# Optimization experiments

Hardware: AMD Instinct MI355X
Metric: run time of the kernel (lower is better)

## Reference

```python
import jax, jax.numpy as jnp
import numpy as np

B, S, D = 1, 1024, 512
HEADS, HID = 8, 64
DH = D // HEADS          # 64
CD = D * DH              # 32768 channels in diagonal block
DT = 0.1


def causal_fft_conv(u, k):
    # u: (..., C, S), k: (C, S) -> causal convolution along last axis
    s = u.shape[-1]
    n = 2 * s
    Uf = jnp.fft.rfft(u, n=n, axis=-1)
    Kf = jnp.fft.rfft(k, n=n, axis=-1)
    return jnp.fft.irfft(Uf * Kf, n=n, axis=-1)[..., :s]


def setup_inputs() -> dict:
    key = jax.random.key(0)
    ks = jax.random.split(key, 10)
    x = jax.random.normal(ks[0], (B, S, D), dtype=jnp.float32)
    sc = 1.0 / np.sqrt(D)
    WQ = jax.random.normal(ks[1], (D, D), dtype=jnp.float32) * sc
    WK = jax.random.normal(ks[2], (D, D), dtype=jnp.float32) * sc
    WV = jax.random.normal(ks[3], (D, D), dtype=jnp.float32) * sc
    WO = jax.random.normal(ks[4], (D, D), dtype=jnp.float32) * sc
    # shift SSM: taps C (A = shift matrix, B = e1) + skip D
    C_shift = jax.random.normal(ks[5], (D, HID), dtype=jnp.float32) / np.sqrt(HID)
    D_shift = jax.random.normal(ks[6], (D,), dtype=jnp.float32)
    # S4D-Inv initialization (deterministic: real_random=imag_random=False)
    n = np.arange(HID, dtype=np.float32)
    A_re = jnp.full((HID,), -0.5, dtype=jnp.float32)
    A_im = jnp.asarray((HID / np.pi) * (HID / (2.0 * n + 1.0) - 1.0), dtype=jnp.float32)
    C_re = jax.random.normal(ks[7], (CD, HID), dtype=jnp.float32) / np.sqrt(HID)
    C_im = jax.random.normal(ks[8], (CD, HID), dtype=jnp.float32) / np.sqrt(HID)
    D_diag = jax.random.normal(ks[9], (CD,), dtype=jnp.float32)
    return {"x": x, "WQ": WQ, "WK": WK, "WV": WV, "WO": WO,
            "C_shift": C_shift, "D_shift": D_shift,
            "A_re": A_re, "A_im": A_im, "C_re": C_re, "C_im": C_im,
            "D_diag": D_diag}


def reference(x, WQ, WK, WV, WO, C_shift, D_shift, A_re, A_im, C_re, C_im, D_diag):
    b, s, d = x.shape
    Q = x @ WQ.T
    K = x @ WK.T
    V = x @ WV.T

    # ---- S4 shift block on K: FIR conv with taps C_shift + skip ----
    k_shift = jnp.pad(C_shift, ((0, 0), (0, s - HID)))  # (D, S)
    Kc = jnp.swapaxes(K, 1, 2)                          # (B, D, S)
    Kc = causal_fft_conv(Kc, k_shift) + D_shift[:, None] * Kc
    K = jnp.swapaxes(Kc, 1, 2)

    # ---- heads ----
    Qh = jnp.swapaxes(Q.reshape(b, s, HEADS, DH), 1, 2)  # (B,H,S,dh)
    Kh = jnp.swapaxes(K.reshape(b, s, HEADS, DH), 1, 2)
    Vh = jnp.swapaxes(V.reshape(b, s, HEADS, DH), 1, 2)

    # KV outer product: (B,H,S,dh,dh)
    KV = Kh[..., :, None] * Vh[..., None, :]
    KVf = jnp.transpose(KV, (0, 2, 1, 3, 4)).reshape(b, s, CD)

    # ---- S4D diagonal block (bilinear disc., convolutional form) ----
    A = A_re + 1j * A_im                                # (N,) complex
    dA = (1.0 + DT * A / 2.0) / (1.0 - DT * A / 2.0)
    dB = DT / (1.0 - DT * A / 2.0)
    logdA = jnp.log(dA)                                 # (N,)
    vand = jnp.exp(jnp.arange(s)[None, :] * logdA[:, None])  # (N, S)
    CB = (C_re + 1j * C_im) * dB[None, :]               # (CD, N)
    Kd = 2.0 * jnp.real(CB @ vand)                      # (CD, S) SSM kernel

    KVc = jnp.swapaxes(KVf, 1, 2)                       # (B, CD, S)
    KVc = causal_fft_conv(KVc, Kd) + D_diag[:, None] * KVc
    KVd = jnp.swapaxes(KVc, 1, 2).reshape(b, s, HEADS, DH, DH)
    KVd = jnp.transpose(KVd, (0, 2, 1, 3, 4))           # (B,H,S,dh,dh)

    # ---- combine with Q and output projection ----
    O = jnp.einsum('bhnc,bhncd->bhnd', Qh, KVd)         # (B,H,S,dh)
    O = jnp.swapaxes(O, 1, 2).reshape(b, s, d)
    return O @ WO.T
```

## Files before the change

### kernel.cpp

```cpp
#include <hip/hip_runtime.h>

#define S 1024
#define D 512
#define HID 64
#define CD 32768
#define DT 0.1f

typedef __attribute__((ext_vector_type(4))) float floatx4;
typedef __attribute__((ext_vector_type(8))) short shortx8;
typedef short shortx8_a __attribute__((ext_vector_type(8), may_alias));
typedef short shortx4_a __attribute__((ext_vector_type(4), may_alias));
typedef unsigned int uint_a __attribute__((may_alias));
typedef unsigned int uint2_a __attribute__((ext_vector_type(2), may_alias));
typedef unsigned int uint4_a __attribute__((ext_vector_type(4), may_alias));
typedef float float4_a __attribute__((ext_vector_type(4), may_alias));
typedef float float_a __attribute__((may_alias));

__device__ __forceinline__ unsigned short f2bf(float f) {
  union { float f; unsigned int u; } v;
  v.f = f;
  unsigned int r = v.u + 0x7FFFu + ((v.u >> 16) & 1u);
  return (unsigned short)(r >> 16);
}
__device__ __forceinline__ float bf2f(unsigned short h) {
  union { unsigned int u; float f; } v;
  v.u = ((unsigned int)h) << 16;
  return v.f;
}
__device__ __forceinline__ void cvt_hilo(float v, unsigned short& h, unsigned short& lo) {
  h = f2bf(v);
  lo = f2bf(v - bf2f(h));
}

__global__ __launch_bounds__(256) void fused_qkv_cbkd(
    const float* __restrict__ x, const float* __restrict__ WQ,
    const float* __restrict__ WK, const float* __restrict__ WV,
    const float* __restrict__ Are, const float* __restrict__ Aim,
    const float* __restrict__ Cre, const float* __restrict__ Cim,
    float* __restrict__ QT, float* __restrict__ KrawT, float* __restrict__ VT,
    unsigned short* __restrict__ cb2pack, unsigned short* __restrict__ kdpack) {
  __shared__ __align__(16) char LB[21760];
  const int tid = threadIdx.x;
  const int bid = blockIdx.x;
  const int l = tid & 63, w = tid >> 6;
  const int l15 = l & 15, q = l >> 4;

  if (bid < 384) {
    unsigned short* Wh = (unsigned short*)LB;
    unsigned short* Wl = Wh + 2560;
    unsigned short* Xh = Wl + 2560;
    unsigned short* Xl = Xh + 2560;
    float_a* Ct = (float_a*)LB;
    const int mat = bid >> 7;
    const int rem = bid & 127;
    const int n0 = (rem & 7) * 64, m0 = (rem >> 3) * 64;
    const float* Wsel = (mat == 0) ? WQ : (mat == 1) ? WK : WV;
    float* CT = (mat == 0) ? QT : (mat == 1) ? KrawT : VT;

    floatx4 acc[4];
#pragma unroll
    for (int nt = 0; nt < 4; ++nt) acc[nt] = (floatx4){0.f, 0.f, 0.f, 0.f};

    for (int k0 = 0; k0 < D; k0 += 32) {
      if (k0) __syncthreads();
#pragma unroll
      for (int p = 0; p < 2; ++p) {
        const int idx = tid + 256 * p;
        const int row = idx >> 3, c4 = (idx & 7) * 4;
        const float4 wv = *(const float4*)&Wsel[(n0 + row) * D + k0 + c4];
        const float4 xv = *(const float4*)&x[(m0 + row) * D + k0 + c4];
        unsigned short h0, h1, h2, h3, g0, g1, g2, g3;
        cvt_hilo(wv.x, h0, g0); cvt_hilo(wv.y, h1, g1);
        cvt_hilo(wv.z, h2, g2); cvt_hilo(wv.w, h3, g3);
        uint2_a hv = {(unsigned int)h0 | ((unsigned int)h1 << 16),
                      (unsigned int)h2 | ((unsigned int)h3 << 16)};
        uint2_a lv = {(unsigned int)g0 | ((unsigned int)g1 << 16),
                      (unsigned int)g2 | ((unsigned int)g3 << 16)};
        *(uint2_a*)&Wh[row * 40 + c4] = hv;
        *(uint2_a*)&Wl[row * 40 + c4] = lv;
        cvt_hilo(xv.x, h0, g0); cvt_hilo(xv.y, h1, g1);
        cvt_hilo(xv.z, h2, g2); cvt_hilo(xv.w, h3, g3);
        uint2_a hv2 = {(unsigned int)h0 | ((unsigned int)h1 << 16),
                       (unsigned int)h2 | ((unsigned int)h3 << 16)};
        uint2_a lv2 = {(unsigned int)g0 | ((unsigned int)g1 << 16),
                       (unsigned int)g2 | ((unsigned int)g3 << 16)};
        *(uint2_a*)&Xh[row * 40 + c4] = hv2;
        *(uint2_a*)&Xl[row * 40 + c4] = lv2;
      }
      __syncthreads();
      const shortx8 xh = *(const shortx8_a*)&Xh[(16 * w + l15) * 40 + 8 * q];
      const shortx8 xl = *(const shortx8_a*)&Xl[(16 * w + l15) * 40 + 8 * q];
#pragma unroll
      for (int nt = 0; nt < 4; ++nt) {
        const shortx8 wh = *(const shortx8_a*)&Wh[(16 * nt + l15) * 40 + 8 * q];
        const shortx8 wl = *(const shortx8_a*)&Wl[(16 * nt + l15) * 40 + 8 * q];
        acc[nt] = __builtin_amdgcn_mfma_f32_16x16x32_bf16(wh, xh, acc[nt], 0, 0, 0);
        acc[nt] = __builtin_amdgcn_mfma_f32_16x16x32_bf16(wh, xl, acc[nt], 0, 0, 0);
        acc[nt] = __builtin_amdgcn_mfma_f32_16x16x32_bf16(wl, xh, acc[nt], 0, 0, 0);
      }
    }
    __syncthreads();
#pragma unroll
    for (int nt = 0; nt < 4; ++nt)
#pragma unroll
      for (int v = 0; v < 4; ++v)
        Ct[(16 * nt + 4 * q + v) * 68 + 16 * w + l15] = acc[nt][v];
    __syncthreads();
#pragma unroll
    for (int p = 0; p < 4; ++p) {
      const int row = (tid >> 4) + 16 * p;
      const int col4 = (tid & 15) * 4;
      *(float4_a*)&CT[(n0 + row) * S + m0 + col4] = *(const float4_a*)&Ct[row * 68 + col4];
    }
  } else {
    unsigned short* cbs = (unsigned short*)LB;
    unsigned short* PCc2s = (unsigned short*)(LB + 4352);
    const int c0 = (bid - 384) << 4;
    {
      const int n = l, seg = w;
      const float ar = Are[n], ai = Aim[n];
      const float den_re = 1.0f - 0.05f * ar;
      const float den_im = -0.05f * ai;
      const float num_re = 1.0f + 0.05f * ar;
      const float num_im = 0.05f * ai;
      const float inv_d2 = 1.0f / (den_re * den_re + den_im * den_im);
      const float dAr = (num_re * den_re + num_im * den_im) * inv_d2;
      const float dAi = (num_im * den_re - num_re * den_im) * inv_d2;
      float e2r = dAr * dAr - dAi * dAi, e2i = 2.0f * dAr * dAi;
      float e4r = e2r * e2r - e2i * e2i, e4i = 2.0f * e2r * e2i;
      float e8r = e4r * e4r - e4i * e4i, e8i = 2.0f * e4r * e4i;
      float e16r = e8r * e8r - e8i * e8i, e16i = 2.0f * e8r * e8i;
      float br = 1.0f, bi = 0.0f;
      for (int sgo = 0; sgo < seg; ++sgo) {
        const float nr = br * e16r - bi * e16i;
        bi = br * e16i + bi * e16r;
        br = nr;
      }
      float pr = br, pi = bi;
      for (int k = 16 * seg + 1; k <= 16 * seg + 16; ++k) {
        const float nr = pr * dAr - pi * dAi;
        pi = pr * dAi + pi * dAr;
        pr = nr;
        if (k <= 63) {
          PCc2s[k * 136 + n] = f2bf(pr);
          PCc2s[k * 136 + 64 + n] = f2bf(-pi);
        }
      }
      if (seg == 0) {
        PCc2s[n] = f2bf(1.0f);
        PCc2s[64 + n] = 0;
      }
    }
#pragma unroll
    for (int ii = 0; ii < 4; ++ii) {
      const int idx = tid + 256 * ii;
      const int ci = idx >> 6, n = idx & 63;
      const int c = c0 + ci;
      const float ar = Are[n], ai = Aim[n];
      const float den_re = 1.0f - 0.05f * ar;
      const float den_im = -0.05f * ai;
      const float inv_d2 = 1.0f / (den_re * den_re + den_im * den_im);
      const float dBr = DT * den_re * inv_d2;
      const float dBi = -DT * den_im * inv_d2;
      const float cr = Cre[c * HID + n], cim = Cim[c * HID + n];
      const unsigned short re = f2bf(2.0f * (cr * dBr - cim * dBi));
      const unsigned short im = f2bf(2.0f * (cr * dBi + cim * dBr));
      cbs[ci * 136 + n] = re;
      cbs[ci * 136 + 64 + n] = im;
      cb2pack[c * 128 + n] = re;
      cb2pack[c * 128 + 64 + n] = im;
    }
    __syncthreads();
    floatx4 acc = {0.f, 0.f, 0.f, 0.f};
#pragma unroll
    for (int k = 0; k < 4; ++k) {
      const shortx8 a = *(const shortx8_a*)&cbs[l15 * 136 + 8 * q + 32 * k];
      const shortx8 b = *(const shortx8_a*)&PCc2s[(16 * w + l15) * 136 + 8 * q + 32 * k];
      acc = __builtin_amdgcn_mfma_f32_16x16x32_bf16(a, b, acc, 0, 0, 0);
    }
    const int dlt = 16 * w + l15;
#pragma unroll
    for (int v = 0; v < 4; ++v)
      kdpack[(c0 + 4 * q + v) * 128 + 64 - dlt] = f2bf(acc[v]);
    const int row = tid >> 4, p = tid & 15;
#pragma unroll
    for (int k2 = 0; k2 < 4; ++k2) {
      const int idx = p + 16 * k2;
      const int m = (idx == 0) ? 0 : 64 + idx;
      kdpack[(c0 + row) * 128 + m] = 0;
    }
  }
}

__global__ __launch_bounds__(256) void shift_ssmT(const float* __restrict__ KrawT,
                                                  const float* __restrict__ Cs,
                                                  const float* __restrict__ Ds,
                                                  float* __restrict__ KnT) {
  __shared__ float kpad[64 + S];
  const int d = blockIdx.x, tid = threadIdx.x;
  if (tid < 64) kpad[tid] = 0.0f;
  *(float4_a*)&kpad[64 + 4 * tid] = *(const float4_a*)&KrawT[d * S + 4 * tid];
  const float dskip = Ds[d];
  const float* taps = Cs + d * HID;
  __syncthreads();
  float acc[4];
#pragma unroll
  for (int s = 0; s < 4; ++s) acc[s] = dskip * kpad[64 + tid + 256 * s];
  for (int j = 0; j < 64; ++j) {
    const float tj = taps[j];
#pragma unroll
    for (int s = 0; s < 4; ++s) acc[s] += tj * kpad[64 + tid + 256 * s - j];
  }
#pragma unroll
  for (int s = 0; s < 4; ++s) KnT[d * S + tid + 256 * s] = acc[s];
}

__global__ __launch_bounds__(256, 2) void s4d_fused(
    const float* __restrict__ KnT, const float* __restrict__ VT,
    const float* __restrict__ QT,
    const float* __restrict__ Are, const float* __restrict__ Aim,
    const unsigned short* __restrict__ cb2pack,
    const unsigned short* __restrict__ kdpack,
    const float* __restrict__ Dd, float* __restrict__ OT) {
  __shared__ __align__(16) unsigned short SHu[18176];
  const int tid = threadIdx.x;
  const int l = tid & 63, w = tid >> 6;
  const int l15 = l & 15, q = l >> 4;
  const int h = blockIdx.x >> 6, j = blockIdx.x & 63;
  const int dv = (h << 6) + j;

  {
    const int n = l, seg = w;
    unsigned short* PAreW = SHu;
    unsigned short* PAimW = SHu + 4608;
    unsigned short* PCcW = SHu + 9216;
    float_a* dA64W = (float_a*)(SHu + 17920);
    const float ar = Are[n], ai = Aim[n];
    const float den_re = 1.0f - 0.05f * ar;
    const float den_im = -0.05f * ai;
    const float num_re = 1.0f + 0.05f * ar;
    const float num_im = 0.05f * ai;
    const float inv_d2 = 1.0f / (den_re * den_re + den_im * den_im);
    const float dAr = (num_re * den_re + num_im * den_im) * inv_d2;
    const float dAi = (num_im * den_re - num_re * den_im) * inv_d2;
    float e2r = dAr * dAr - dAi * dAi, e2i = 2.0f * dAr * dAi;
    float e4r = e2r * e2r - e2i * e2i, e4i = 2.0f * e2r * e2i;
    float e8r = e4r * e4r - e4i * e4i, e8i = 2.0f * e4r * e4i;
    float e16r = e8r * e8r - e8i * e8i, e16i = 2.0f * e8r * e8i;
    float br = 1.0f, bi = 0.0f;
    for (int sgo = 0; sgo < seg; ++sgo) {
      const float nr = br * e16r - bi * e16i;
      bi = br * e16i + bi * e16r;
      br = nr;
    }
    float pr = br, pi = bi;
    for (int k = 16 * seg + 1; k <= 16 * seg + 16; ++k) {
      const float nr = pr * dAr - pi * dAi;
      pi = pr * dAi + pi * dAr;
      pr = nr;
      if (k <= 63) {
        PAreW[n * 72 + 63 - k] = f2bf(pr);
        PAimW[n * 72 + 63 - k] = f2bf(pi);
      }
      PCcW[(k - 1) * 136 + 2 * n] = f2bf(pr);
      PCcW[(k - 1) * 136 + 2 * n + 1] = f2bf(-pi);
      if (k == 64) {
        dA64W[2 * n] = pr;
        dA64W[2 * n + 1] = pi;
      }
    }
    if (seg == 0) {
      PAreW[n * 72 + 63] = f2bf(1.0f);
      PAimW[n * 72 + 63] = 0;
    }
  }
  float4 vvr[4];
#pragma unroll
  for (int s = 0; s < 4; ++s)
    vvr[s] = *(const float4*)&VT[dv * S + 4 * l + 256 * s];

  float c2r, c2i, dd;
  unsigned int kdv;
  {
    const int c = (h << 12) + (w << 6) + j;
    c2r = bf2f(cb2pack[c * 128 + l]);
    c2i = bf2f(cb2pack[c * 128 + 64 + l]);
    kdv = *(const uint_a*)&kdpack[c * 128 + 2 * l];
    dd = Dd[c];
  }
  __syncthreads();

  const unsigned short* PAre = SHu;
  const unsigned short* PAim = SHu + 4608;
  const unsigned short* PCc = SHu + 9216;
  const float_a* dA64v = (const float_a*)(SHu + 17920);
  const float er = dA64v[2 * l], ei = dA64v[2 * l + 1];
  shortx8 paR[4][2], paI[4][2];
#pragma unroll
  for (int tt = 0; tt < 4; ++tt) {
    const int rowb = (tt * 16 + l15) * 72 + 8 * q;
    paR[tt][0] = *(const shortx8_a*)&PAre[rowb];
    paR[tt][1] = *(const shortx8_a*)&PAre[rowb + 32];
    paI[tt][0] = *(const shortx8_a*)&PAim[rowb];
    paI[tt][1] = *(const shortx8_a*)&PAim[rowb + 32];
  }
  shortx8 pcb[4][4];
#pragma unroll
  for (int k = 0; k < 4; ++k)
#pragma unroll
    for (int tt = 0; tt < 4; ++tt)
      pcb[k][tt] = *(const shortx8_a*)&PCc[(tt * 16 + l15) * 136 + 8 * q + 32 * k];
  __syncthreads();

  unsigned short* WB = SHu + w * 4048;
  unsigned short* Ub = WB;
  unsigned short* SXY = WB + 1152;
  uint_a* kdR32 = (uint_a*)(WB + 3328);
  unsigned short* kdSH = WB + 3472;

  floatx4 OaccD[4];
  float4 Odd[4];
#pragma unroll
  for (int tt = 0; tt < 4; ++tt) OaccD[tt] = (floatx4){0.f, 0.f, 0.f, 0.f};
#pragma unroll
  for (int s = 0; s < 4; ++s) Odd[s] = make_float4(0.f, 0.f, 0.f, 0.f);

#pragma unroll 1
  for (int it = 0; it < 16; ++it) {
    float nc2r = 0.f, nc2i = 0.f, ndd = 0.f;
    unsigned int nkdv = 0;
    if (it < 15) {
      const int c = (h << 12) + (((it + 1) * 4 + w) << 6) + j;
      nc2r = bf2f(cb2pack[c * 128 + l]);
      nc2i = bf2f(cb2pack[c * 128 + 64 + l]);
      nkdv = *(const uint_a*)&kdpack[c * 128 + 2 * l];
      ndd = Dd[c];
    }
    const int dk = (h << 6) + it * 4 + w;
    const int kb = dk * S + 4 * l;
    float4 kx[4], qtv[4];
#pragma unroll
    for (int s = 0; s < 4; ++s) {
      kx[s] = *(const float4*)&KnT[kb + 256 * s];
      qtv[s] = *(const float4*)&QT[kb + 256 * s];
    }

    kdR32[l] = kdv;
    if (l < 4) kdR32[64 + l] = 0;
    asm volatile("" ::: "memory");
#pragma unroll
    for (int s2 = 0; s2 < 4; ++s2) {
      unsigned int v;
      if (s2 == 0) {
        v = kdR32[l];
      } else if (s2 == 1) {
        v = (kdR32[l] >> 16) | (kdR32[l + 1] << 16);
      } else if (s2 == 2) {
        v = kdR32[l + 1];
      } else {
        v = (kdR32[l + 1] >> 16) | (kdR32[l + 2] << 16);
      }
      *(uint_a*)&kdSH[s2 * 136 + 2 * l] = v;
    }
    asm volatile("" ::: "memory");

#pragma unroll
    for (int s = 0; s < 4; ++s) {
      const int t = 4 * l + 256 * s;
      const int g = t >> 6, r = t & 63;
      const float ux = kx[s].x * vvr[s].x;
      const float uy = kx[s].y * vvr[s].y;
      const float uz = kx[s].z * vvr[s].z;
      const float uw = kx[s].w * vvr[s].w;
      uint2_a pp;
      pp.x = (unsigned int)f2bf(ux) | ((unsigned int)f2bf(uy) << 16);
      pp.y = (unsigned int)f2bf(uz) | ((unsigned int)f2bf(uw) << 16);
      *(uint2_a*)&Ub[g * 72 + r] = pp;
      Odd[s].x += dd * qtv[s].x * ux;
      Odd[s].y += dd * qtv[s].y * uy;
      Odd[s].z += dd * qtv[s].z * uz;
      Odd[s].w += dd * qtv[s].w * uw;
    }
    asm volatile("" ::: "memory");

    const shortx8 b0 = *(const shortx8_a*)&Ub[l15 * 72 + 8 * q];
    const shortx8 b1 = *(const shortx8_a*)&Ub[l15 * 72 + 8 * q + 32];
#pragma unroll
    for (int tt = 0; tt < 4; ++tt) {
      floatx4 z = {0.f, 0.f, 0.f, 0.f};
      floatx4 sre = __builtin_amdgcn_mfma_f32_16x16x32_bf16(paR[tt][0], b0, z, 0, 0, 0);
      sre = __builtin_amdgcn_mfma_f32_16x16x32_bf16(paR[tt][1], b1, sre, 0, 0, 0);
      floatx4 sim = __builtin_amdgcn_mfma_f32_16x16x32_bf16(paI[tt][0], b0, z, 0, 0, 0);
      sim = __builtin_amdgcn_mfma_f32_16x16x32_bf16(paI[tt][1], b1, sim, 0, 0, 0);
      uint4_a wv;
      wv[0] = (unsigned int)f2bf(sre[0]) | ((unsigned int)f2bf(sim[0]) << 16);
      wv[1] = (unsigned int)f2bf(sre[1]) | ((unsigned int)f2bf(sim[1]) << 16);
      wv[2] = (unsigned int)f2bf(sre[2]) | ((unsigned int)f2bf(sim[2]) << 16);
      wv[3] = (unsigned int)f2bf(sre[3]) | ((unsigned int)f2bf(sim[3]) << 16);
      *(uint4_a*)&SXY[l15 * 136 + 32 * tt + 8 * q] = wv;
    }
    asm volatile("" ::: "memory");

    {
      unsigned int rdv[16];
#pragma unroll
      for (int g = 0; g < 16; ++g) rdv[g] = *(const uint_a*)&SXY[g * 136 + 2 * l];
      float xr = 0.f, xi = 0.f;
#pragma unroll
      for (int g = 0; g < 16; ++g) {
        *(uint_a*)&SXY[g * 136 + 2 * l] =
            (unsigned int)f2bf(c2r * xr - c2i * xi) |
            ((unsigned int)f2bf(c2r * xi + c2i * xr) << 16);
        union { unsigned int u; float f; } lo, hi;
        lo.u = rdv[g] << 16;
        hi.u = rdv[g] & 0xffff0000u;
        const float nr = er * xr - ei * xi + lo.f;
        xi = er * xi + ei * xr + hi.f;
        xr = nr;
      }
    }
    asm volatile("" ::: "memory");

    float qD[16];
    {
      const int qb = dk * S + 256 * q + l15;
#pragma unroll
      for (int tt = 0; tt < 4; ++tt)
#pragma unroll
        for (int v = 0; v < 4; ++v)
          qD[4 * tt + v] = QT[qb + 64 * v + 16 * tt];
    }

    floatx4 acc[4];
#pragma unroll
    for (int tt = 0; tt < 4; ++tt) acc[tt] = (floatx4){0.f, 0.f, 0.f, 0.f};
#pragma unroll
    for (int k = 0; k < 4; ++k) {
      const shortx8 xa = *(const shortx8_a*)&SXY[l15 * 136 + 8 * q + 32 * k];
#pragma unroll
      for (int tt = 0; tt < 4; ++tt)
        acc[tt] = __builtin_amdgcn_mfma_f32_16x16x32_bf16(xa, pcb[k][tt], acc[tt], 0, 0, 0);
    }
#pragma unroll
    for (int k = 0; k < 2; ++k) {
      const shortx8 ua = (k == 0) ? b0 : b1;
#pragma unroll
      for (int tt = 0; tt < 4; ++tt) {
        const int r = tt * 16 + l15;
        const int sSh = (4 - (r & 3)) & 3;
        const int addr = sSh * 136 + (64 - r - sSh) + 8 * q + 32 * k;
        const shortx4_a lo = *(const shortx4_a*)&kdSH[addr];
        const shortx4_a hi = *(const shortx4_a*)&kdSH[addr + 4];
        const shortx8 kb8 = __builtin_shufflevector(lo, hi, 0, 1, 2, 3, 4, 5, 6, 7);
        acc[tt] = __builtin_amdgcn_mfma_f32_16x16x32_bf16(ua, kb8, acc[tt], 0, 0, 0);
      }
    }
#pragma unroll
    for (int tt = 0; tt < 4; ++tt)
#pragma unroll
      for (int v = 0; v < 4; ++v)
        OaccD[tt][v] += qD[4 * tt + v] * acc[tt][v];
    c2r = nc2r; c2i = nc2i; kdv = nkdv; dd = ndd;
  }

  asm volatile("" ::: "memory");
  {
    float_a* Ored = (float_a*)WB;
#pragma unroll
    for (int tt = 0; tt < 4; ++tt)
#pragma unroll
      for (int v = 0; v < 4; ++v)
        Ored[256 * q + 64 * v + 16 * tt + l15 + q] = OaccD[tt][v];
    asm volatile("" ::: "memory");
    float4 Oa[4];
#pragma unroll
    for (int s = 0; s < 4; ++s) {
      const float4_a y4 = *(const float4_a*)&Ored[4 * l + 257 * s];
      Oa[s].x = y4.x + Odd[s].x;
      Oa[s].y = y4.y + Odd[s].y;
      Oa[s].z = y4.z + Odd[s].z;
      Oa[s].w = y4.w + Odd[s].w;
    }
    asm volatile("" ::: "memory");
#pragma unroll
    for (int s = 0; s < 4; ++s) {
      float4_a vv = {Oa[s].x, Oa[s].y, Oa[s].z, Oa[s].w};
      *(float4_a*)&Ored[4 * l + 256 * s] = vv;
    }
  }
  __syncthreads();
  {
    const int tq = 256 * w + 4 * l;
    float4_a acc = {0.f, 0.f, 0.f, 0.f};
#pragma unroll
    for (int w2 = 0; w2 < 4; ++w2) {
      const float_a* Ow2 = (const float_a*)(SHu + w2 * 4048);
      acc += *(const float4_a*)&Ow2[tq];
    }
    *(float4_a*)&OT[dv * S + tq] = acc;
  }
}

__global__ __launch_bounds__(256) void gemm_outT(const float* __restrict__ OT,
                                                 const float* __restrict__ WO,
                                                 float* __restrict__ out) {
  __shared__ __align__(16) char LB[20480];
  unsigned short* Wh = (unsigned short*)LB;
  unsigned short* Wl = Wh + 2560;
  unsigned short* Xh = Wl + 2560;
  unsigned short* Xl = Xh + 2560;
  float_a* Ct = (float_a*)LB;
  const int tid = threadIdx.x;
  const int l = tid & 63, w = tid >> 6;
  const int l15 = l & 15, q = l >> 4;
  const int n0 = (blockIdx.x & 7) * 64, m0 = (blockIdx.x >> 3) * 64;

  floatx4 acc[4];
#pragma unroll
  for (int nt = 0; nt < 4; ++nt) acc[nt] = (floatx4){0.f, 0.f, 0.f, 0.f};

  for (int k0 = 0; k0 < D; k0 += 32) {
    if (k0) __syncthreads();
#pragma unroll
    for (int p = 0; p < 2; ++p) {
      const int idx = tid + 256 * p;
      {
        const int row = idx >> 3, c4 = (idx & 7) * 4;
        const float4 wv = *(const float4*)&WO[(n0 + row) * D + k0 + c4];
        unsigned short h0, h1, h2, h3, g0, g1, g2, g3;
        cvt_hilo(wv.x, h0, g0); cvt_hilo(wv.y, h1, g1);
        cvt_hilo(wv.z, h2, g2); cvt_hilo(wv.w, h3, g3);
        uint2_a hv = {(unsigned int)h0 | ((unsigned int)h1 << 16),
                      (unsigned int)h2 | ((unsigned int)h3 << 16)};
        uint2_a lv = {(unsigned int)g0 | ((unsigned int)g1 << 16),
                      (unsigned int)g2 | ((unsigned int)g3 << 16)};
        *(uint2_a*)&Wh[row * 40 + c4] = hv;
        *(uint2_a*)&Wl[row * 40 + c4] = lv;
      }
      {
        const int kk = idx >> 4, m4 = (idx & 15) * 4;
        const float4 ov = *(const float4*)&OT[(k0 + kk) * S + m0 + m4];
        unsigned short h, g;
        cvt_hilo(ov.x, h, g); Xh[(m4 + 0) * 40 + kk] = h; Xl[(m4 + 0) * 40 + kk] = g;
        cvt_hilo(ov.y, h, g); Xh[(m4 + 1) * 40 + kk] = h; Xl[(m4 + 1) * 40 + kk] = g;
        cvt_hilo(ov.z, h, g); Xh[(m4 + 2) * 40 + kk] = h; Xl[(m4 + 2) * 40 + kk] = g;
        cvt_hilo(ov.w, h, g); Xh[(m4 + 3) * 40 + kk] = h; Xl[(m4 + 3) * 40 + kk] = g;
      }
    }
    __syncthreads();
    const shortx8 xh = *(const shortx8_a*)&Xh[(16 * w + l15) * 40 + 8 * q];
    const shortx8 xl = *(const shortx8_a*)&Xl[(16 * w + l15) * 40 + 8 * q];
#pragma unroll
    for (int nt = 0; nt < 4; ++nt) {
      const shortx8 wh = *(const shortx8_a*)&Wh[(16 * nt + l15) * 40 + 8 * q];
      const shortx8 wl = *(const shortx8_a*)&Wl[(16 * nt + l15) * 40 + 8 * q];
      acc[nt] = __builtin_amdgcn_mfma_f32_16x16x32_bf16(wh, xh, acc[nt], 0, 0, 0);
      acc[nt] = __builtin_amdgcn_mfma_f32_16x16x32_bf16(wh, xl, acc[nt], 0, 0, 0);
      acc[nt] = __builtin_amdgcn_mfma_f32_16x16x32_bf16(wl, xh, acc[nt], 0, 0, 0);
    }
  }
  __syncthreads();
#pragma unroll
  for (int nt = 0; nt < 4; ++nt)
#pragma unroll
    for (int v = 0; v < 4; ++v)
      Ct[(16 * w + l15) * 68 + 16 * nt + 4 * q + v] = acc[nt][v];
  __syncthreads();
#pragma unroll
  for (int p = 0; p < 4; ++p) {
    const int row = (tid >> 4) + 16 * p;
    const int col4 = (tid & 15) * 4;
    *(float4_a*)&out[(m0 + row) * D + n0 + col4] = *(const float4_a*)&Ct[row * 68 + col4];
  }
}

extern "C" void kernel_launch(void* const* d_in, const int* in_sizes, int n_in,
                              void* d_out, int out_size, void* d_ws, size_t ws_size,
                              hipStream_t stream) {
  const float* x   = (const float*)d_in[0];
  const float* WQ  = (const float*)d_in[1];
  const float* WK  = (const float*)d_in[2];
  const float* WV  = (const float*)d_in[3];
  const float* WO  = (const float*)d_in[4];
  const float* Cs  = (const float*)d_in[5];
  const float* Ds  = (const float*)d_in[6];
  const float* Are = (const float*)d_in[7];
  const float* Aim = (const float*)d_in[8];
  const float* Cre = (const float*)d_in[9];
  const float* Cim = (const float*)d_in[10];
  const float* Dd  = (const float*)d_in[11];
  float* out = (float*)d_out;

  char* ws = (char*)d_ws;
  const size_t SD = (size_t)S * D * 4;
  float* QT    = (float*)(ws + 0 * SD);
  float* KrawT = (float*)(ws + 1 * SD);
  float* VT    = (float*)(ws + 2 * SD);
  float* KnT   = (float*)(ws + 3 * SD);
  float* OT    = (float*)(ws + 4 * SD);
  unsigned short* cb2pack = (unsigned short*)(ws + 5 * SD);
  unsigned short* kdpack  = (unsigned short*)(ws + 5 * SD + 8388608);

  fused_qkv_cbkd<<<384 + CD / 16, 256, 0, stream>>>(
      x, WQ, WK, WV, Are, Aim, Cre, Cim, QT, KrawT, VT, cb2pack, kdpack);
  shift_ssmT<<<512, 256, 0, stream>>>(KrawT, Cs, Ds, KnT);
  s4d_fused<<<512, 256, 0, stream>>>(KnT, VT, QT, Are, Aim, cb2pack, kdpack, Dd, OT);
  gemm_outT<<<128, 256, 0, stream>>>(OT, WO, out);
}
```

Baseline: 186.7 us.

## Split s4d_fused channel reduction across two blocks and sum partials in output GEMM

Each output row of s4d_fused is now computed by two blocks, each covering half of the 64 key channels, giving 1024 blocks instead of 512. The two partial results go to separate buffers (the second reuses the KrawT workspace, which is dead by then), and gemm_outT adds them while loading its input tile. The launch bound is raised to 4 blocks per CU to fit more waves. In exchange, each block repeats the per-block setup (discretization tables, V loads), and the GEMM reads twice as much input.

```diff
diff --git a/kernel.cpp b/kernel.cpp
--- a/kernel.cpp
+++ b/kernel.cpp
@@ -215,19 +215,22 @@
   for (int s = 0; s < 4; ++s) KnT[d * S + tid + 256 * s] = acc[s];
 }
 
-__global__ __launch_bounds__(256, 2) void s4d_fused(
+__global__ __launch_bounds__(256, 4) void s4d_fused(
     const float* __restrict__ KnT, const float* __restrict__ VT,
     const float* __restrict__ QT,
     const float* __restrict__ Are, const float* __restrict__ Aim,
     const unsigned short* __restrict__ cb2pack,
     const unsigned short* __restrict__ kdpack,
-    const float* __restrict__ Dd, float* __restrict__ OT) {
+    const float* __restrict__ Dd, float* __restrict__ OT,
+    float* __restrict__ OT1) {
   __shared__ __align__(16) unsigned short SHu[18176];
   const int tid = threadIdx.x;
   const int l = tid & 63, w = tid >> 6;
   const int l15 = l & 15, q = l >> 4;
-  const int h = blockIdx.x >> 6, j = blockIdx.x & 63;
-  const int dv = (h << 6) + j;
+  const int half = blockIdx.x & 1;
+  const int dv = blockIdx.x >> 1;
+  const int h = dv >> 6, j = dv & 63;
+  float* __restrict__ OTout = half ? OT1 : OT;
 
   {
     const int n = l, seg = w;
@@ -282,7 +285,7 @@
   float c2r, c2i, dd;
   unsigned int kdv;
   {
-    const int c = (h << 12) + (w << 6) + j;
+    const int c = (h << 12) + ((half * 32 + w) << 6) + j;
     c2r = bf2f(cb2pack[c * 128 + l]);
     c2i = bf2f(cb2pack[c * 128 + 64 + l]);
     kdv = *(const uint_a*)&kdpack[c * 128 + 2 * l];
@@ -326,17 +329,17 @@
   for (int s = 0; s < 4; ++s) Odd[s] = make_float4(0.f, 0.f, 0.f, 0.f);
 
 #pragma unroll 1
-  for (int it = 0; it < 16; ++it) {
+  for (int itl = 0; itl < 8; ++itl) {
     float nc2r = 0.f, nc2i = 0.f, ndd = 0.f;
     unsigned int nkdv = 0;
-    if (it < 15) {
-      const int c = (h << 12) + (((it + 1) * 4 + w) << 6) + j;
+    if (itl < 7) {
+      const int c = (h << 12) + ((half * 32 + (itl + 1) * 4 + w) << 6) + j;
       nc2r = bf2f(cb2pack[c * 128 + l]);
       nc2i = bf2f(cb2pack[c * 128 + 64 + l]);
       nkdv = *(const uint_a*)&kdpack[c * 128 + 2 * l];
       ndd = Dd[c];
     }
-    const int dk = (h << 6) + it * 4 + w;
+    const int dk = (h << 6) + half * 32 + itl * 4 + w;
     const int kb = dk * S + 4 * l;
     float4 kx[4], qtv[4];
 #pragma unroll
@@ -497,11 +500,12 @@
       const float_a* Ow2 = (const float_a*)(SHu + w2 * 4048);
       acc += *(const float4_a*)&Ow2[tq];
     }
-    *(float4_a*)&OT[dv * S + tq] = acc;
+    *(float4_a*)&OTout[dv * S + tq] = acc;
   }
 }
 
 __global__ __launch_bounds__(256) void gemm_outT(const float* __restrict__ OT,
+                                                 const float* __restrict__ OT1,
                                                  const float* __restrict__ WO,
                                                  float* __restrict__ out) {
   __shared__ __align__(16) char LB[20480];
@@ -539,7 +543,10 @@
       }
       {
         const int kk = idx >> 4, m4 = (idx & 15) * 4;
-        const float4 ov = *(const float4*)&OT[(k0 + kk) * S + m0 + m4];
+        const float4 o0 = *(const float4*)&OT[(k0 + kk) * S + m0 + m4];
+        const float4 o1 = *(const float4*)&OT1[(k0 + kk) * S + m0 + m4];
+        const float4 ov = make_float4(o0.x + o1.x, o0.y + o1.y,
+                                      o0.z + o1.z, o0.w + o1.w);
         unsigned short h, g;
         cvt_hilo(ov.x, h, g); Xh[(m4 + 0) * 40 + kk] = h; Xl[(m4 + 0) * 40 + kk] = g;
         cvt_hilo(ov.y, h, g); Xh[(m4 + 1) * 40 + kk] = h; Xl[(m4 + 1) * 40 + kk] = g;
@@ -598,12 +605,13 @@
   float* VT    = (float*)(ws + 2 * SD);
   float* KnT   = (float*)(ws + 3 * SD);
   float* OT    = (float*)(ws + 4 * SD);
+  float* OT1   = KrawT;
   unsigned short* cb2pack = (unsigned short*)(ws + 5 * SD);
   unsigned short* kdpack  = (unsigned short*)(ws + 5 * SD + 8388608);
 
   fused_qkv_cbkd<<<384 + CD / 16, 256, 0, stream>>>(
       x, WQ, WK, WV, Are, Aim, Cre, Cim, QT, KrawT, VT, cb2pack, kdpack);
   shift_ssmT<<<512, 256, 0, stream>>>(KrawT, Cs, Ds, KnT);
-  s4d_fused<<<512, 256, 0, stream>>>(KnT, VT, QT, Are, Aim, cb2pack, kdpack, Dd, OT);
-  gemm_outT<<<128, 256, 0, stream>>>(OT, WO, out);
-}
+  s4d_fused<<<1024, 256, 0, stream>>>(KnT, VT, QT, Are, Aim, cb2pack, kdpack, Dd, OT, OT1);
+  gemm_outT<<<128, 256, 0, stream>>>(OT, OT1, WO, out);
+}
```

Result: slower. 337.8 us (+80.9%).
